# Performance work log

Measured on AMD Instinct MI355X. Metric: run time of the kernel, lower is better.

The kernel has to match this reference:

```python
import jax, jax.numpy as jnp
import numpy as np

GROUPS = 8
NUM_HEADS = 8
EPS = 1e-5


def setup_inputs() -> dict:
    key = jax.random.key(0)
    ks = jax.random.split(key, 3)
    C = 512
    x = jax.random.normal(ks[0], (2, C, 64, 64), dtype=jnp.float32)
    norm_w = jnp.ones((C,), jnp.float32)
    norm_b = jnp.zeros((C,), jnp.float32)
    qkv_w = jax.random.normal(ks[1], (3 * C, C), dtype=jnp.float32) * (C ** -0.5)
    qkv_b = jnp.zeros((3 * C,), jnp.float32)
    proj_w = jax.random.normal(ks[2], (C, C), dtype=jnp.float32) * (C ** -0.5)
    proj_b = jnp.zeros((C,), jnp.float32)
    return {"x": x, "norm_w": norm_w, "norm_b": norm_b,
            "qkv_w": qkv_w, "qkv_b": qkv_b,
            "proj_w": proj_w, "proj_b": proj_b}


def reference(x, norm_w, norm_b, qkv_w, qkv_b, proj_w, proj_b):
    b, c, h, w = x.shape
    n = h * w
    hd = c // NUM_HEADS

    # GroupNorm(8, c): normalize over (channels-in-group, h, w)
    xg = x.reshape(b, GROUPS, c // GROUPS, h, w)
    mean = jnp.mean(xg, axis=(2, 3, 4), keepdims=True)
    var = jnp.var(xg, axis=(2, 3, 4), keepdims=True)
    xg = (xg - mean) * jax.lax.rsqrt(var + EPS)
    x_norm = xg.reshape(b, c, h, w) * norm_w[None, :, None, None] + norm_b[None, :, None, None]

    x_flat = x_norm.reshape(b, c, n)  # (b, c, n)
    # 1x1 Conv1d == channel-wise linear
    qkv = jnp.einsum('oc,bcn->bon', qkv_w, x_flat) + qkv_b[None, :, None]
    q, k, v = jnp.split(qkv, 3, axis=1)
    q = q.reshape(b, NUM_HEADS, hd, n)
    k = k.reshape(b, NUM_HEADS, hd, n)
    v = v.reshape(b, NUM_HEADS, hd, n)

    attn = jnp.einsum('bhdn,bhdm->bhnm', q, k) * (hd ** -0.5)  # (b,h,n,n)
    attn = jax.nn.softmax(attn, axis=-1)
    out = jnp.einsum('bhnm,bhdm->bhdn', attn, v).reshape(b, c, n)

    out = jnp.einsum('oc,bcn->bon', proj_w, out) + proj_b[None, :, None]
    return x + out.reshape(b, c, h, w)
```

## Files before the change

### kernel.cpp

```cpp
#include <hip/hip_runtime.h>
#include <stdint.h>

#define B_   2
#define C_   512
#define N_   4096
#define G_   8
#define NH_  8
#define HD_  64
#define GRPELEMS ((C_ / G_) * N_)
#define NCHUNK 16

typedef __bf16 bf16x8 __attribute__((ext_vector_type(8)));
typedef float  f32x4  __attribute__((ext_vector_type(4)));

#if __has_builtin(__builtin_amdgcn_exp2f)
#define EXP2(x) __builtin_amdgcn_exp2f(x)
#else
#define EXP2(x) exp2f(x)
#endif

__device__ inline unsigned f2bf(float f) {
    union { float f; unsigned u; } v; v.f = f;
    return (v.u + 0x7FFFu + ((v.u >> 16) & 1u)) >> 16;
}
__device__ inline __bf16 tobf(float f) {
    unsigned short u = (unsigned short)f2bf(f);
    union { unsigned short u; __bf16 b; } c; c.u = u;
    return c.b;
}
__device__ inline unsigned pktrunc(float f0, float f1) {
    return __builtin_amdgcn_perm(__float_as_uint(f1), __float_as_uint(f0),
                                 0x07060302u);
}
__device__ inline float trunc_bf(float f) {
    return __uint_as_float(__float_as_uint(f) & 0xffff0000u);
}

#define GLOAD16(g, l)                                                     \
    __builtin_amdgcn_global_load_lds(                                     \
        (const __attribute__((address_space(1))) unsigned*)(g),           \
        (__attribute__((address_space(3))) unsigned*)(l), 16, 0, 0)

__global__ __launch_bounds__(256) void prep(const float* __restrict__ x,
                                            const float* __restrict__ qw,
                                            const float* __restrict__ pw,
                                            float* __restrict__ psum,
                                            float* __restrict__ psq,
                                            __bf16* __restrict__ dq,
                                            __bf16* __restrict__ dp) {
    const int blk = blockIdx.x;
    const int t = threadIdx.x;
    if (blk < 256) {
        const float4* p = (const float4*)x + (size_t)blk * 4096;
        float s = 0.f, s2 = 0.f;
#pragma unroll
        for (int i = 0; i < 16; ++i) {
            float4 v = p[t + (i << 8)];
            s  += v.x + v.y + v.z + v.w;
            s2 += v.x * v.x + v.y * v.y + v.z * v.z + v.w * v.w;
        }
#pragma unroll
        for (int off = 1; off < 64; off <<= 1) {
            s  += __shfl_xor(s, off);
            s2 += __shfl_xor(s2, off);
        }
        __shared__ float rs[4], rq[4];
        if ((t & 63) == 0) { rs[t >> 6] = s; rq[t >> 6] = s2; }
        __syncthreads();
        if (t == 0) {
            psum[blk] = rs[0] + rs[1] + rs[2] + rs[3];
            psq[blk]  = rq[0] + rq[1] + rq[2] + rq[3];
        }
    } else {
        const int QW4 = (3 * C_ * C_) / 4;
        int idx = (blk - 256) * 256 + t;
        float4 v; __bf16* dst; int o;
        if (idx < QW4) { v = ((const float4*)qw)[idx]; dst = dq; o = idx; }
        else           { v = ((const float4*)pw)[idx - QW4]; dst = dp; o = idx - QW4; }
        uint2 pk;
        pk.x = f2bf(v.x) | (f2bf(v.y) << 16);
        pk.y = f2bf(v.z) | (f2bf(v.w) << 16);
        *(uint2*)(dst + (size_t)o * 4) = pk;
    }
}

__global__ __launch_bounds__(256) void gn_apply_t(const float* __restrict__ x,
                                                  const float* __restrict__ w,
                                                  const float* __restrict__ bb,
                                                  const float* __restrict__ psum,
                                                  const float* __restrict__ psq,
                                                  __bf16* __restrict__ xnT) {
    const int p0 = blockIdx.x << 6, c0 = blockIdx.y << 6, b = blockIdx.z;
    __shared__ __bf16 T[64][76];
    __shared__ float red[2 * NCHUNK];
    __shared__ float smr[2];
    const int tid = threadIdx.x;
    const int bg = b * G_ + (c0 >> 6);

    if (tid < NCHUNK)            red[tid] = psum[bg * NCHUNK + tid];
    else if (tid < 2 * NCHUNK)   red[tid] = psq[bg * NCHUNK + tid - NCHUNK];
    __syncthreads();
    if (tid == 0) {
        float s = 0.f, q = 0.f;
#pragma unroll
        for (int i = 0; i < NCHUNK; ++i) { s += red[i]; q += red[NCHUNK + i]; }
        const float inv = 1.f / (float)GRPELEMS;
        float mean = s * inv;
        float var  = q * inv - mean * mean;
        smr[0] = mean;
        smr[1] = rsqrtf(var + 1e-5f);
    }
    __syncthreads();
    const float mean = smr[0], rstd = smr[1];

    const int tr  = tid >> 4;
    const int tc4 = (tid & 15) << 2;
    const float* xb = x + ((size_t)b * C_ + c0) * N_ + p0;
#pragma unroll
    for (int cc = tr; cc < 64; cc += 16) {
        int c = c0 + cc;
        float sc = rstd * w[c];
        float sh = bb[c] - mean * sc;
        float4 v = *(const float4*)(xb + (size_t)cc * N_ + tc4);
        T[tc4 + 0][cc] = tobf(v.x * sc + sh);
        T[tc4 + 1][cc] = tobf(v.y * sc + sh);
        T[tc4 + 2][cc] = tobf(v.z * sc + sh);
        T[tc4 + 3][cc] = tobf(v.w * sc + sh);
    }
    __syncthreads();
    __bf16* dst = xnT + ((size_t)b * N_ + p0) * C_ + c0;
#pragma unroll
    for (int pp = tr; pp < 64; pp += 16)
        *(uint2*)(dst + (size_t)pp * C_ + tc4) = *(const uint2*)&T[pp][tc4];
}

template <int M_TOTAL, int EPI>
__global__ __launch_bounds__(256) void gemm_bf16(const __bf16* __restrict__ A,
                                                 const __bf16* __restrict__ Bm,
                                                 const float* __restrict__ bias,
                                                 const float* __restrict__ resid,
                                                 __bf16* __restrict__ qT,
                                                 __bf16* __restrict__ kP,
                                                 __bf16* __restrict__ vP,
                                                 float* __restrict__ Y) {
    const int b  = blockIdx.z;
    const int M0 = blockIdx.y << 6;
    const int N0 = blockIdx.x << 7;
    const int tid = threadIdx.x;
    const int w = tid >> 6, lane = tid & 63;
    const int quad = lane >> 4, l16 = lane & 15;
    const int wr = w >> 1, wc = w & 1;

    __shared__ __bf16 As[64 * 64];
    __shared__ __bf16 Bs[128 * 64];

    const __bf16* Bb = Bm + (size_t)b * ((size_t)N_ * C_);

    const int srow = lane >> 3;
    const int sg   = lane & 7;

    f32x4 acc[2][4];
#pragma unroll
    for (int mt = 0; mt < 2; ++mt)
#pragma unroll
        for (int nt = 0; nt < 4; ++nt) acc[mt][nt] = (f32x4){0.f, 0.f, 0.f, 0.f};

    for (int k0 = 0; k0 < C_; k0 += 64) {
        __syncthreads();
#pragma unroll
        for (int i = 0; i < 2; ++i) {
            int r  = (w << 4) + (i << 3) + srow;
            int gc = ((sg ^ (r & 7)) << 3);
            GLOAD16(A + (size_t)(M0 + r) * C_ + k0 + gc, As + (((w << 1) + i) << 9));
        }
#pragma unroll
        for (int i = 0; i < 4; ++i) {
            int r  = (w << 5) + (i << 3) + srow;
            int gc = ((sg ^ (r & 7)) << 3);
            GLOAD16(Bb + (size_t)(N0 + r) * C_ + k0 + gc, Bs + (((w << 2) + i) << 9));
        }
        __syncthreads();

#pragma unroll
        for (int kk = 0; kk < 2; ++kk) {
            bf16x8 af[2], bfr[4];
            const int gk = (kk << 2) + quad;
#pragma unroll
            for (int mt = 0; mt < 2; ++mt) {
                int m = (wr << 5) + (mt << 4) + l16;
                af[mt] = *(const bf16x8*)&As[(m << 6) + ((gk ^ (m & 7)) << 3)];
            }
#pragma unroll
            for (int nt = 0; nt < 4; ++nt) {
                int n = (wc << 6) + (nt << 4) + l16;
                bfr[nt] = *(const bf16x8*)&Bs[(n << 6) + ((gk ^ (n & 7)) << 3)];
            }
#pragma unroll
            for (int mt = 0; mt < 2; ++mt)
#pragma unroll
                for (int nt = 0; nt < 4; ++nt)
                    acc[mt][nt] = __builtin_amdgcn_mfma_f32_16x16x32_bf16(
                        af[mt], bfr[nt], acc[mt][nt], 0, 0, 0);
        }
    }

    if (EPI == 0) {
        const int t = M0 >> 9;
        const float sc = (t == 0) ? (0.125f * 1.44269504f) : 1.f;
#pragma unroll
        for (int mt = 0; mt < 2; ++mt) {
            const int o0 = M0 + (wr << 5) + (mt << 4) + (quad << 2);
            const int h  = (o0 >> 6) & 7;
            const int d0 = o0 & 63;
            const size_t bh = (size_t)b * NH_ + h;
            float bi[4];
#pragma unroll
            for (int r = 0; r < 4; ++r) bi[r] = bias[o0 + r];
            if (t == 0) {
                __bf16* dst = qT + (bh * N_) * HD_ + d0;
#pragma unroll
                for (int nt = 0; nt < 4; ++nt) {
                    int p = N0 + (wc << 6) + (nt << 4) + l16;
                    f32x4 v = acc[mt][nt];
                    uint2 pk;
                    pk.x = f2bf((v[0] + bi[0]) * sc) | (f2bf((v[1] + bi[1]) * sc) << 16);
                    pk.y = f2bf((v[2] + bi[2]) * sc) | (f2bf((v[3] + bi[3]) * sc) << 16);
                    *(uint2*)(dst + (size_t)p * HD_) = pk;
                }
            } else if (t == 1) {
                __bf16* dst = kP + bh * ((size_t)N_ * HD_);
                const size_t kkbase = (size_t)(d0 >> 3) * N_;
                const int rem = d0 & 7;
#pragma unroll
                for (int nt = 0; nt < 4; ++nt) {
                    int p = N0 + (wc << 6) + (nt << 4) + l16;
                    f32x4 v = acc[mt][nt];
                    uint2 pk;
                    pk.x = f2bf(v[0] + bi[0]) | (f2bf(v[1] + bi[1]) << 16);
                    pk.y = f2bf(v[2] + bi[2]) | (f2bf(v[3] + bi[3]) << 16);
                    *(uint2*)(dst + (kkbase + p) * 8 + rem) = pk;
                }
            } else {
                __bf16* dst = vP + bh * ((size_t)HD_ * N_);
#pragma unroll
                for (int nt = 0; nt < 4; ++nt) {
                    int p = N0 + (wc << 6) + (nt << 4) + l16;
                    const size_t gb2 = ((size_t)(p >> 3) * HD_) * 8 + (p & 7);
                    f32x4 v = acc[mt][nt];
#pragma unroll
                    for (int r = 0; r < 4; ++r)
                        dst[gb2 + (size_t)(d0 + r) * 8] = tobf(v[r] + bi[r]);
                }
            }
        }
    } else {
#pragma unroll
        for (int mt = 0; mt < 2; ++mt) {
            const int o0 = M0 + (wr << 5) + (mt << 4) + (quad << 2);
            float bi[4];
#pragma unroll
            for (int r = 0; r < 4; ++r) bi[r] = bias[o0 + r];
#pragma unroll
            for (int nt = 0; nt < 4; ++nt) {
                int p = N0 + (wc << 6) + (nt << 4) + l16;
                f32x4 v = acc[mt][nt];
#pragma unroll
                for (int r = 0; r < 4; ++r) {
                    size_t off = ((size_t)b * C_ + o0 + r) * N_ + p;
                    Y[off] = v[r] + bi[r] + resid[off];
                }
            }
        }
    }
}

__global__ __launch_bounds__(256) void attn_mfma(const __bf16* __restrict__ qT,
                                                 const __bf16* __restrict__ kP,
                                                 const __bf16* __restrict__ vP,
                                                 __bf16* __restrict__ attT) {
    const int tid  = threadIdx.x;
    const int w    = tid >> 6;
    const int lane = tid & 63;
    const int quad = lane >> 4;
    const int l16  = lane & 15;
    const int l7   = l16 & 7;
    const int h = blockIdx.y, b = blockIdx.z;
    const int qw0 = (blockIdx.x << 7) + (w << 5);

    __shared__ __bf16 Ps[4][32][64];

    const size_t bh = (size_t)b * NH_ + h;
    const __bf16* qTb = qT + bh * ((size_t)N_ * HD_);
    const __bf16* kPb = kP + bh * ((size_t)N_ * HD_);
    const __bf16* vPb = vP + bh * ((size_t)HD_ * N_);

    bf16x8 qf[2][2];
#pragma unroll
    for (int qt = 0; qt < 2; ++qt)
#pragma unroll
        for (int hh = 0; hh < 2; ++hh)
            qf[qt][hh] = *(const bf16x8*)(qTb +
                (size_t)(qw0 + (qt << 4) + l16) * HD_ + (hh << 5) + (quad << 3));

#define KADDR(hh, kt, kb) (kPb + (((size_t)((hh << 2) + quad) * N_) + (kb) + ((kt) << 4) + l16) * 8)
#define VADDR(h2, dt, kb) (vPb + (((size_t)(((kb) >> 3) + ((h2) << 2) + quad) * HD_) + ((dt) << 4) + l16) * 8)

    const f32x4 zero4 = {0.f, 0.f, 0.f, 0.f};
    f32x4 o[4][2];
#pragma unroll
    for (int dt = 0; dt < 4; ++dt) { o[dt][0] = zero4; o[dt][1] = zero4; }
    float lacc[2] = {0.f, 0.f};

    bf16x8 kf[2][4];
#pragma unroll
    for (int hh = 0; hh < 2; ++hh)
#pragma unroll
        for (int kt = 0; kt < 4; ++kt)
            kf[hh][kt] = *(const bf16x8*)KADDR(hh, kt, 0);

    for (int it = 0; it < 64; ++it) {
        const int kb = it << 6;

        bf16x8 vf[2][4];
#pragma unroll
        for (int h2 = 0; h2 < 2; ++h2)
#pragma unroll
            for (int dt = 0; dt < 4; ++dt)
                vf[h2][dt] = *(const bf16x8*)VADDR(h2, dt, kb);

        f32x4 s[4][2];
#pragma unroll
        for (int kt = 0; kt < 4; ++kt) { s[kt][0] = zero4; s[kt][1] = zero4; }
#pragma unroll
        for (int hh = 0; hh < 2; ++hh)
#pragma unroll
            for (int kt = 0; kt < 4; ++kt) {
                s[kt][0] = __builtin_amdgcn_mfma_f32_16x16x32_bf16(
                    kf[hh][kt], qf[0][hh], s[kt][0], 0, 0, 0);
                s[kt][1] = __builtin_amdgcn_mfma_f32_16x16x32_bf16(
                    kf[hh][kt], qf[1][hh], s[kt][1], 0, 0, 0);
            }

#pragma unroll
        for (int qt = 0; qt < 2; ++qt)
#pragma unroll
            for (int kt = 0; kt < 4; ++kt) {
                f32x4 sv = s[kt][qt];
                float e0 = EXP2(sv[0]), e1 = EXP2(sv[1]);
                float e2 = EXP2(sv[2]), e3 = EXP2(sv[3]);
                lacc[qt] += (trunc_bf(e0) + trunc_bf(e1)) +
                            (trunc_bf(e2) + trunc_bf(e3));
                uint2 pk;
                pk.x = pktrunc(e0, e1);
                pk.y = pktrunc(e2, e3);
                *(uint2*)&Ps[w][(qt << 4) + l16]
                            [(((kt << 2) + quad) ^ (l7 << 1)) << 2] = pk;
            }

        if (it < 63) {
#pragma unroll
            for (int hh = 0; hh < 2; ++hh)
#pragma unroll
                for (int kt = 0; kt < 4; ++kt)
                    kf[hh][kt] = *(const bf16x8*)KADDR(hh, kt, kb + 64);
        }

#pragma unroll
        for (int hh = 0; hh < 2; ++hh) {
            bf16x8 pf0 = *(const bf16x8*)&Ps[w][l16]
                          [(((hh << 3) + (quad << 1)) ^ (l7 << 1)) << 2];
            bf16x8 pf1 = *(const bf16x8*)&Ps[w][16 + l16]
                          [(((hh << 3) + (quad << 1)) ^ (l7 << 1)) << 2];
#pragma unroll
            for (int dt = 0; dt < 4; ++dt) {
                o[dt][0] = __builtin_amdgcn_mfma_f32_16x16x32_bf16(
                    vf[hh][dt], pf0, o[dt][0], 0, 0, 0);
                o[dt][1] = __builtin_amdgcn_mfma_f32_16x16x32_bf16(
                    vf[hh][dt], pf1, o[dt][1], 0, 0, 0);
            }
        }
    }

    float lq[2];
#pragma unroll
    for (int qt = 0; qt < 2; ++qt) {
        float v = lacc[qt];
        v += __shfl_xor(v, 16);
        v += __shfl_xor(v, 32);
        lq[qt] = v;
    }

#pragma unroll
    for (int qt = 0; qt < 2; ++qt) {
        float inv = 1.f / lq[qt];
        int n = qw0 + (qt << 4) + l16;
        __bf16* dst = attT + ((size_t)b * N_ + n) * C_ + h * HD_ + (quad << 2);
#pragma unroll
        for (int dt = 0; dt < 4; ++dt) {
            uint2 pk;
            pk.x = f2bf(o[dt][qt][0] * inv) | (f2bf(o[dt][qt][1] * inv) << 16);
            pk.y = f2bf(o[dt][qt][2] * inv) | (f2bf(o[dt][qt][3] * inv) << 16);
            *(uint2*)(dst + (dt << 4)) = pk;
        }
    }
#undef KADDR
#undef VADDR
}

extern "C" void kernel_launch(void* const* d_in, const int* in_sizes, int n_in,
                              void* d_out, int out_size, void* d_ws, size_t ws_size,
                              hipStream_t stream) {
    const float* x      = (const float*)d_in[0];
    const float* norm_w = (const float*)d_in[1];
    const float* norm_b = (const float*)d_in[2];
    const float* qkv_w  = (const float*)d_in[3];
    const float* qkv_b  = (const float*)d_in[4];
    const float* proj_w = (const float*)d_in[5];
    const float* proj_b = (const float*)d_in[6];
    float* out = (float*)d_out;

    const size_t BCN = (size_t)B_ * C_ * N_;
    float* psum  = (float*)d_ws;
    float* psq   = psum + 256;
    __bf16* xnT  = (__bf16*)(psq + 256);
    __bf16* qT   = xnT + BCN;
    __bf16* kP   = qT + BCN;
    __bf16* vP   = kP + BCN;
    __bf16* attT = vP + BCN;
    __bf16* wq   = attT + BCN;
    __bf16* wp   = wq + (size_t)3 * C_ * C_;

    prep<<<1280, 256, 0, stream>>>(x, qkv_w, proj_w, psum, psq, wq, wp);
    gn_apply_t<<<dim3(N_ / 64, C_ / 64, B_), 256, 0, stream>>>(
        x, norm_w, norm_b, psum, psq, xnT);
    gemm_bf16<3 * C_, 0><<<dim3(N_ / 128, 3 * C_ / 64, B_), 256, 0, stream>>>(
        wq, xnT, qkv_b, nullptr, qT, kP, vP, nullptr);
    attn_mfma<<<dim3(N_ / 128, NH_, B_), 256, 0, stream>>>(qT, kP, vP, attT);
    gemm_bf16<C_, 1><<<dim3(N_ / 128, C_ / 64, B_), 256, 0, stream>>>(
        wp, attT, proj_b, x, nullptr, nullptr, nullptr, out);
}
```

Baseline: 209.5 us.

## Software-pipeline QK^T scores one tile ahead with double-buffered K fragments

Result: slower. 309.7 us (+47.9%).

```diff
diff --git a/kernel.cpp b/kernel.cpp
--- a/kernel.cpp
+++ b/kernel.cpp
@@ -274,10 +274,10 @@
     }
 }
 
-__global__ __launch_bounds__(256) void attn_mfma(const __bf16* __restrict__ qT,
-                                                 const __bf16* __restrict__ kP,
-                                                 const __bf16* __restrict__ vP,
-                                                 __bf16* __restrict__ attT) {
+__global__ __launch_bounds__(256, 2) void attn_mfma(const __bf16* __restrict__ qT,
+                                                    const __bf16* __restrict__ kP,
+                                                    const __bf16* __restrict__ vP,
+                                                    __bf16* __restrict__ attT) {
     const int tid  = threadIdx.x;
     const int w    = tid >> 6;
     const int lane = tid & 63;
@@ -311,75 +311,100 @@
     for (int dt = 0; dt < 4; ++dt) { o[dt][0] = zero4; o[dt][1] = zero4; }
     float lacc[2] = {0.f, 0.f};
 
-    bf16x8 kf[2][4];
+    bf16x8 kfA[2][4], kfB[2][4];
 #pragma unroll
     for (int hh = 0; hh < 2; ++hh)
 #pragma unroll
-        for (int kt = 0; kt < 4; ++kt)
-            kf[hh][kt] = *(const bf16x8*)KADDR(hh, kt, 0);
-
-    for (int it = 0; it < 64; ++it) {
-        const int kb = it << 6;
-
-        bf16x8 vf[2][4];
-#pragma unroll
-        for (int h2 = 0; h2 < 2; ++h2)
-#pragma unroll
-            for (int dt = 0; dt < 4; ++dt)
-                vf[h2][dt] = *(const bf16x8*)VADDR(h2, dt, kb);
-
-        f32x4 s[4][2];
-#pragma unroll
-        for (int kt = 0; kt < 4; ++kt) { s[kt][0] = zero4; s[kt][1] = zero4; }
-#pragma unroll
-        for (int hh = 0; hh < 2; ++hh)
-#pragma unroll
-            for (int kt = 0; kt < 4; ++kt) {
-                s[kt][0] = __builtin_amdgcn_mfma_f32_16x16x32_bf16(
-                    kf[hh][kt], qf[0][hh], s[kt][0], 0, 0, 0);
-                s[kt][1] = __builtin_amdgcn_mfma_f32_16x16x32_bf16(
-                    kf[hh][kt], qf[1][hh], s[kt][1], 0, 0, 0);
-            }
-
-#pragma unroll
-        for (int qt = 0; qt < 2; ++qt)
-#pragma unroll
-            for (int kt = 0; kt < 4; ++kt) {
-                f32x4 sv = s[kt][qt];
-                float e0 = EXP2(sv[0]), e1 = EXP2(sv[1]);
-                float e2 = EXP2(sv[2]), e3 = EXP2(sv[3]);
-                lacc[qt] += (trunc_bf(e0) + trunc_bf(e1)) +
-                            (trunc_bf(e2) + trunc_bf(e3));
-                uint2 pk;
-                pk.x = pktrunc(e0, e1);
-                pk.y = pktrunc(e2, e3);
-                *(uint2*)&Ps[w][(qt << 4) + l16]
-                            [(((kt << 2) + quad) ^ (l7 << 1)) << 2] = pk;
-            }
-
-        if (it < 63) {
-#pragma unroll
-            for (int hh = 0; hh < 2; ++hh)
-#pragma unroll
-                for (int kt = 0; kt < 4; ++kt)
-                    kf[hh][kt] = *(const bf16x8*)KADDR(hh, kt, kb + 64);
-        }
-
-#pragma unroll
-        for (int hh = 0; hh < 2; ++hh) {
-            bf16x8 pf0 = *(const bf16x8*)&Ps[w][l16]
-                          [(((hh << 3) + (quad << 1)) ^ (l7 << 1)) << 2];
-            bf16x8 pf1 = *(const bf16x8*)&Ps[w][16 + l16]
-                          [(((hh << 3) + (quad << 1)) ^ (l7 << 1)) << 2];
-#pragma unroll
-            for (int dt = 0; dt < 4; ++dt) {
-                o[dt][0] = __builtin_amdgcn_mfma_f32_16x16x32_bf16(
-                    vf[hh][dt], pf0, o[dt][0], 0, 0, 0);
-                o[dt][1] = __builtin_amdgcn_mfma_f32_16x16x32_bf16(
-                    vf[hh][dt], pf1, o[dt][1], 0, 0, 0);
-            }
-        }
-    }
+        for (int kt = 0; kt < 4; ++kt) {
+            kfA[hh][kt] = *(const bf16x8*)KADDR(hh, kt, 0);
+            kfB[hh][kt] = *(const bf16x8*)KADDR(hh, kt, 64);
+        }
+
+    f32x4 sA[4][2], sB[4][2];
+#pragma unroll
+    for (int kt = 0; kt < 4; ++kt) { sA[kt][0] = zero4; sA[kt][1] = zero4; }
+#pragma unroll
+    for (int hh = 0; hh < 2; ++hh)
+#pragma unroll
+        for (int kt = 0; kt < 4; ++kt) {
+            sA[kt][0] = __builtin_amdgcn_mfma_f32_16x16x32_bf16(
+                kfA[hh][kt], qf[0][hh], sA[kt][0], 0, 0, 0);
+            sA[kt][1] = __builtin_amdgcn_mfma_f32_16x16x32_bf16(
+                kfA[hh][kt], qf[1][hh], sA[kt][1], 0, 0, 0);
+        }
+
+#define AITER(IT, S_CUR, S_NXT, KF_LD, KF_CMP, DO_LOAD, DO_SNXT)             \
+    {                                                                        \
+        const int kb = (IT) << 6;                                            \
+        bf16x8 vf[2][4];                                                     \
+        _Pragma("unroll")                                                    \
+        for (int h2 = 0; h2 < 2; ++h2)                                       \
+            _Pragma("unroll")                                                \
+            for (int dt = 0; dt < 4; ++dt)                                   \
+                vf[h2][dt] = *(const bf16x8*)VADDR(h2, dt, kb);              \
+        if (DO_LOAD) {                                                       \
+            _Pragma("unroll")                                                \
+            for (int hh = 0; hh < 2; ++hh)                                   \
+                _Pragma("unroll")                                            \
+                for (int kt = 0; kt < 4; ++kt)                               \
+                    KF_LD[hh][kt] = *(const bf16x8*)KADDR(hh, kt, kb + 128); \
+        }                                                                    \
+          \
+        _Pragma("unroll")                                                    \
+        for (int qt = 0; qt < 2; ++qt)                                       \
+            _Pragma("unroll")                                                \
+            for (int kt = 0; kt < 4; ++kt) {                                 \
+                f32x4 sv = S_CUR[kt][qt];                                    \
+                float e0 = EXP2(sv[0]), e1 = EXP2(sv[1]);                    \
+                float e2 = EXP2(sv[2]), e3 = EXP2(sv[3]);                    \
+                lacc[qt] += (trunc_bf(e0) + trunc_bf(e1)) +                  \
+                            (trunc_bf(e2) + trunc_bf(e3));                   \
+                uint2 pk;                                                    \
+                pk.x = pktrunc(e0, e1);                                      \
+                pk.y = pktrunc(e2, e3);                                      \
+                *(uint2*)&Ps[w][(qt << 4) + l16]                             \
+                            [(((kt << 2) + quad) ^ (l7 << 1)) << 2] = pk;    \
+            }                                                                \
+            \
+        if (DO_SNXT) {                                                       \
+            _Pragma("unroll")                                                \
+            for (int kt = 0; kt < 4; ++kt) {                                 \
+                S_NXT[kt][0] = zero4; S_NXT[kt][1] = zero4;                  \
+            }                                                                \
+            _Pragma("unroll")                                                \
+            for (int hh = 0; hh < 2; ++hh)                                   \
+                _Pragma("unroll")                                            \
+                for (int kt = 0; kt < 4; ++kt) {                             \
+                    S_NXT[kt][0] = __builtin_amdgcn_mfma_f32_16x16x32_bf16(  \
+                        KF_CMP[hh][kt], qf[0][hh], S_NXT[kt][0], 0, 0, 0);   \
+                    S_NXT[kt][1] = __builtin_amdgcn_mfma_f32_16x16x32_bf16(  \
+                        KF_CMP[hh][kt], qf[1][hh], S_NXT[kt][1], 0, 0, 0);   \
+                }                                                            \
+        }                                                                    \
+                                                 \
+        _Pragma("unroll")                                                    \
+        for (int hh = 0; hh < 2; ++hh) {                                     \
+            bf16x8 pf0 = *(const bf16x8*)&Ps[w][l16]                         \
+                          [(((hh << 3) + (quad << 1)) ^ (l7 << 1)) << 2];    \
+            bf16x8 pf1 = *(const bf16x8*)&Ps[w][16 + l16]                    \
+                          [(((hh << 3) + (quad << 1)) ^ (l7 << 1)) << 2];    \
+            _Pragma("unroll")                                                \
+            for (int dt = 0; dt < 4; ++dt) {                                 \
+                o[dt][0] = __builtin_amdgcn_mfma_f32_16x16x32_bf16(          \
+                    vf[hh][dt], pf0, o[dt][0], 0, 0, 0);                     \
+                o[dt][1] = __builtin_amdgcn_mfma_f32_16x16x32_bf16(          \
+                    vf[hh][dt], pf1, o[dt][1], 0, 0, 0);                     \
+            }                                                                \
+        }                                                                    \
+    }
+
+    for (int m = 0; m < 31; ++m) {
+        AITER((m << 1),       sA, sB, kfA, kfB, true,  true);
+        AITER(((m << 1) + 1), sB, sA, kfB, kfA, true,  true);
+    }
+    AITER(62, sA, sB, kfA, kfB, false, true);
+    AITER(63, sB, sA, kfB, kfA, false, false);
+#undef AITER
 
     float lq[2];
 #pragma unroll
```

## Split attention key range across wave pairs and merge partials in LDS

Applied to the files above, without the earlier changes.

New measurement: 625.7 us. 2.99x slower.

```diff
diff --git a/kernel.cpp b/kernel.cpp
--- a/kernel.cpp
+++ b/kernel.cpp
@@ -274,10 +274,10 @@
     }
 }
 
-__global__ __launch_bounds__(256) void attn_mfma(const __bf16* __restrict__ qT,
-                                                 const __bf16* __restrict__ kP,
-                                                 const __bf16* __restrict__ vP,
-                                                 __bf16* __restrict__ attT) {
+__global__ __launch_bounds__(512, 4) void attn_mfma(const __bf16* __restrict__ qT,
+                                                    const __bf16* __restrict__ kP,
+                                                    const __bf16* __restrict__ vP,
+                                                    __bf16* __restrict__ attT) {
     const int tid  = threadIdx.x;
     const int w    = tid >> 6;
     const int lane = tid & 63;
@@ -285,9 +285,12 @@
     const int l16  = lane & 15;
     const int l7   = l16 & 7;
     const int h = blockIdx.y, b = blockIdx.z;
-    const int qw0 = (blockIdx.x << 7) + (w << 5);
-
-    __shared__ __bf16 Ps[4][32][64];
+    const int p    = w >> 1;
+    const int half = w & 1;
+    const int qw0 = (blockIdx.x << 7) + (p << 5);
+
+    __shared__ __align__(16) float smemf[4 * 32 * 68 + 4 * 2 * 16];
+    __bf16 (*Ps)[32][64] = (__bf16(*)[32][64])smemf;
 
     const size_t bh = (size_t)b * NH_ + h;
     const __bf16* qTb = qT + bh * ((size_t)N_ * HD_);
@@ -311,14 +314,16 @@
     for (int dt = 0; dt < 4; ++dt) { o[dt][0] = zero4; o[dt][1] = zero4; }
     float lacc[2] = {0.f, 0.f};
 
+    const int it0 = half << 5;
+
     bf16x8 kf[2][4];
 #pragma unroll
     for (int hh = 0; hh < 2; ++hh)
 #pragma unroll
         for (int kt = 0; kt < 4; ++kt)
-            kf[hh][kt] = *(const bf16x8*)KADDR(hh, kt, 0);
-
-    for (int it = 0; it < 64; ++it) {
+            kf[hh][kt] = *(const bf16x8*)KADDR(hh, kt, it0 << 6);
+
+    for (int it = it0; it < it0 + 32; ++it) {
         const int kb = it << 6;
 
         bf16x8 vf[2][4];
@@ -357,7 +362,7 @@
                             [(((kt << 2) + quad) ^ (l7 << 1)) << 2] = pk;
             }
 
-        if (it < 63) {
+        if (it < it0 + 31) {
 #pragma unroll
             for (int hh = 0; hh < 2; ++hh)
 #pragma unroll
@@ -390,17 +395,38 @@
         lq[qt] = v;
     }
 
-#pragma unroll
-    for (int qt = 0; qt < 2; ++qt) {
-        float inv = 1.f / lq[qt];
-        int n = qw0 + (qt << 4) + l16;
-        __bf16* dst = attT + ((size_t)b * N_ + n) * C_ + h * HD_ + (quad << 2);
-#pragma unroll
-        for (int dt = 0; dt < 4; ++dt) {
-            uint2 pk;
-            pk.x = f2bf(o[dt][qt][0] * inv) | (f2bf(o[dt][qt][1] * inv) << 16);
-            pk.y = f2bf(o[dt][qt][2] * inv) | (f2bf(o[dt][qt][3] * inv) << 16);
-            *(uint2*)(dst + (dt << 4)) = pk;
+    float (*Om)[32][68] = (float(*)[32][68])smemf;
+    float (*Lm)[2][16]  = (float(*)[2][16])(smemf + 4 * 32 * 68);
+
+    __syncthreads();
+    if (half == 1) {
+#pragma unroll
+        for (int qt = 0; qt < 2; ++qt)
+#pragma unroll
+            for (int dt = 0; dt < 4; ++dt)
+                *(f32x4*)&Om[p][(qt << 4) + l16][(dt << 4) + (quad << 2)] =
+                    o[dt][qt];
+        if (quad == 0) { Lm[p][0][l16] = lq[0]; Lm[p][1][l16] = lq[1]; }
+    }
+    __syncthreads();
+    if (half == 0) {
+#pragma unroll
+        for (int qt = 0; qt < 2; ++qt) {
+            float inv = 1.f / (lq[qt] + Lm[p][qt][l16]);
+            int n = qw0 + (qt << 4) + l16;
+            __bf16* dst = attT + ((size_t)b * N_ + n) * C_ + h * HD_ + (quad << 2);
+#pragma unroll
+            for (int dt = 0; dt < 4; ++dt) {
+                f32x4 po = *(const f32x4*)&Om[p][(qt << 4) + l16]
+                                            [(dt << 4) + (quad << 2)];
+                f32x4 ov = o[dt][qt];
+                uint2 pk;
+                pk.x = f2bf((ov[0] + po[0]) * inv) |
+                       (f2bf((ov[1] + po[1]) * inv) << 16);
+                pk.y = f2bf((ov[2] + po[2]) * inv) |
+                       (f2bf((ov[3] + po[3]) * inv) << 16);
+                *(uint2*)(dst + (dt << 4)) = pk;
+            }
         }
     }
 #undef KADDR
@@ -435,7 +461,7 @@
         x, norm_w, norm_b, psum, psq, xnT);
     gemm_bf16<3 * C_, 0><<<dim3(N_ / 128, 3 * C_ / 64, B_), 256, 0, stream>>>(
         wq, xnT, qkv_b, nullptr, qT, kP, vP, nullptr);
-    attn_mfma<<<dim3(N_ / 128, NH_, B_), 256, 0, stream>>>(qT, kP, vP, attT);
+    attn_mfma<<<dim3(N_ / 128, NH_, B_), 512, 0, stream>>>(qT, kP, vP, attT);
     gemm_bf16<C_, 1><<<dim3(N_ / 128, C_ / 64, B_), 256, 0, stream>>>(
         wp, attT, proj_b, x, nullptr, nullptr, nullptr, out);
 }
```
